# Kernel optimization log

Hardware: AMD Instinct MI355X
Metric: run time of the kernel (lower is better)

The kernel has to match this reference:

```python
import jax, jax.numpy as jnp
import numpy as np

B, S, H, NH = 2, 2048, 1024, 16
HD = H // NH
SCALE = float(H) ** 0.5  # note: source scales by sqrt(hidden_dim), not sqrt(head_dim)
EPS = 1e-5


def setup_inputs() -> dict:
    key = jax.random.key(0)
    ks = jax.random.split(key, 16)
    s = 0.02
    return {
        "q": jax.random.normal(ks[0], (B, S, H), jnp.float32),
        "k": jax.random.normal(ks[1], (B, S, H), jnp.float32),
        "v": jax.random.normal(ks[2], (B, S, H), jnp.float32),
        "mask": jax.random.randint(ks[3], (B, 1, S, S), 0, 2, jnp.int32),
        "Wq": jax.random.normal(ks[4], (H, H), jnp.float32) * s,
        "bq": jnp.zeros((H,), jnp.float32),
        "Wk": jax.random.normal(ks[5], (H, H), jnp.float32) * s,
        "bk": jnp.zeros((H,), jnp.float32),
        "Wv": jax.random.normal(ks[6], (H, H), jnp.float32) * s,
        "bv": jnp.zeros((H,), jnp.float32),
        "Wfc": jax.random.normal(ks[7], (H, H), jnp.float32) * s,
        "bfc": jnp.zeros((H,), jnp.float32),
        "gamma": jnp.ones((H,), jnp.float32),
        "beta": jnp.zeros((H,), jnp.float32),
    }


def reference(q, k, v, mask, Wq, bq, Wk, bk, Wv, bv, Wfc, bfc, gamma, beta):
    residual = q
    qh = (q @ Wq + bq).reshape(B, S, NH, HD)
    kh = (k @ Wk + bk).reshape(B, S, NH, HD)
    vh = (v @ Wv + bv).reshape(B, S, NH, HD)
    # full [B, NH, S, S] score matrix, as in the source
    energy = jnp.einsum('nqhd,nkhd->nhqk', qh, kh)
    energy = jnp.where(mask == 0, jnp.float32(-1e9), energy)
    attn = jax.nn.softmax(energy / SCALE, axis=3)  # dropout p=0.0 -> identity
    out = jnp.einsum('nhqk,nkhd->nqhd', attn, vh).reshape(B, S, H)
    y = out @ Wfc + bfc + residual
    mu = jnp.mean(y, axis=-1, keepdims=True)
    var = jnp.mean((y - mu) ** 2, axis=-1, keepdims=True)
    return gamma * (y - mu) / jnp.sqrt(var + EPS) + beta
```

## Files before the change

kernel.cpp:

```cpp
#include <hip/hip_runtime.h>
#include <hip/hip_bf16.h>

#define S_LEN  2048
#define HDIM   1024
#define NHEADS 16
#define HEADD  64
#define BATCH  2
#define MTOT   (BATCH * S_LEN)
#define K2EXP  0.04508422f

typedef __attribute__((ext_vector_type(8)))  __bf16 bf16x8;
typedef __attribute__((ext_vector_type(4)))  __bf16 bf16x4;
typedef __attribute__((ext_vector_type(4)))  float  f32x4;
typedef __attribute__((ext_vector_type(16))) float  f32x16;

__device__ __forceinline__ void gload16(const void* g, void* l) {
  __builtin_amdgcn_global_load_lds(
      (const __attribute__((address_space(1))) void*)g,
      (__attribute__((address_space(3))) void*)l, 16, 0, 0);
}
template<int STRIDE>
__device__ __forceinline__ bf16x8 lds_rdS(const __bf16* base, int row, int bcol) {
  const char* p = (const char*)base + row * STRIDE + (bcol ^ ((row & (STRIDE / 16 - 1)) << 4));
  return *(const bf16x8*)p;
}
__device__ __forceinline__ unsigned cvtpk_bf16(float lo, float hi) {
  unsigned r;
  asm("v_cvt_pk_bf16_f32 %0, %1, %2" : "=v"(r) : "v"(lo), "v"(hi));
  return r;
}
__device__ __forceinline__ void plswap(unsigned& a, unsigned& b) {
  asm volatile("v_permlane32_swap_b32 %0, %1" : "+v"(a), "+v"(b));
}

__global__ __launch_bounds__(256)
void prologue_kernel(const float* __restrict__ q, const float* __restrict__ k,
                     const float* __restrict__ v, const int* __restrict__ mask,
                     const float* __restrict__ Wq, const float* __restrict__ Wk,
                     const float* __restrict__ Wv, const float* __restrict__ Wfc,
                     __bf16* __restrict__ Qc, __bf16* __restrict__ Kc,
                     __bf16* __restrict__ Vc, unsigned* __restrict__ mbH,
                     __bf16* __restrict__ Wt)
{
  __shared__ float T[64][65];
  const int id = blockIdx.x;
  const int tid = threadIdx.x;
  if (id < 6144) {
    const int z = id >> 11, blk = id & 2047;
    const float* src = (z == 0) ? q : (z == 1) ? k : v;
    __bf16* dst = (z == 0) ? Qc : (z == 1) ? Kc : Vc;
    const size_t i = ((size_t)blk * 256 + tid) * 8;
    const float4 a = *(const float4*)&src[i];
    const float4 c = *(const float4*)&src[i + 4];
    bf16x8 o;
    o[0] = (__bf16)a.x; o[1] = (__bf16)a.y; o[2] = (__bf16)a.z; o[3] = (__bf16)a.w;
    o[4] = (__bf16)c.x; o[5] = (__bf16)c.y; o[6] = (__bf16)c.z; o[7] = (__bf16)c.w;
    *(bf16x8*)&dst[i] = o;
  } else if (id < 38912) {
    const size_t idx = (size_t)(id - 6144) * 256 + tid;
    const int m = mask[idx];
    const unsigned long long bal = __ballot(m != 0);
    const int lane = tid & 63;
    if ((lane & 31) == 0) {
      const int hh = lane >> 5;
      unsigned wlo = 0, whi = 0;
      #pragma unroll
      for (int j = 0; j < 16; ++j) {
        const int kvl = (j & 3) + 8 * (j >> 2) + 4 * hh;
        wlo |= (unsigned)((bal >> kvl) & 1ULL) << j;
        whi |= (unsigned)((bal >> (32 + kvl)) & 1ULL) << j;
      }
      const int b   = (int)(idx >> 22);
      const int qq  = (int)(idx >> 11) & 2047;
      const int seg = ((int)idx & 2047) >> 6;
      mbH[(((size_t)(hh * 2 + b)) * 32 + seg) * S_LEN + qq] = wlo | (whi << 16);
    }
  } else {
    const int f = id - 38912;
    const int z = f >> 8;
    const float* W = (z == 0) ? Wq : (z == 1) ? Wk : (z == 2) ? Wv : Wfc;
    const float sc = (z == 0) ? K2EXP : 1.0f;
    __bf16* O = Wt + (size_t)z * HDIM * HDIM;
    const int k0 = ((f >> 4) & 15) * 64, n0 = (f & 15) * 64;
    const int r  = tid >> 4;
    const int c4 = (tid & 15) * 4;
    #pragma unroll
    for (int p = 0; p < 4; ++p) {
      const int row = r + p * 16;
      const float4 vv = *(const float4*)&W[(size_t)(k0 + row) * HDIM + n0 + c4];
      T[row][c4 + 0] = vv.x; T[row][c4 + 1] = vv.y;
      T[row][c4 + 2] = vv.z; T[row][c4 + 3] = vv.w;
    }
    __syncthreads();
    #pragma unroll
    for (int p = 0; p < 4; ++p) {
      const int n = r + p * 16;
      bf16x4 o;
      #pragma unroll
      for (int i = 0; i < 4; ++i) o[i] = (__bf16)(T[c4 + i][n] * sc);
      *(bf16x4*)&O[(size_t)(n0 + n) * HDIM + k0 + c4] = o;
    }
  }
}

template<int MODE, int BMT>
__device__ __forceinline__ void gemm_body(
    __bf16* As, __bf16* Bs,
    const __bf16* __restrict__ A, const __bf16* __restrict__ Wt,
    const float* __restrict__ bias, float bscale,
    const float* __restrict__ resid,
    __bf16* __restrict__ Ob, float* __restrict__ Of, __bf16* __restrict__ Vtg)
{
  constexpr int AI = BMT / 32;
  const int tid = threadIdx.x, lane = tid & 63, w = tid >> 6;
  const int fr = lane & 15, k8 = (lane >> 4) * 8;
  const int wr = w >> 1, wc = w & 1;
  const int f   = blockIdx.x + gridDim.x * blockIdx.y;
  const int cpx = (gridDim.x * gridDim.y) >> 3;
  const int fs  = (f & 7) * cpx + (f >> 3);
  const int m0 = (fs / gridDim.x) * BMT, n0 = (fs % gridDim.x) * 128;
  const int srow8 = lane >> 3, slot = lane & 7;

  f32x4 acc[AI][4] = {};

  #define G_STAGE(kt, bf)                                                    \
    {                                                                        \
      _Pragma("unroll")                                                      \
      for (int c = 0; c < AI; ++c) {                                         \
        const int ra = w * (BMT / 4) + c * 8 + srow8;                        \
        gload16(&A[(size_t)(m0 + ra) * HDIM + (kt) * 64 + ((slot ^ (ra & 7)) * 8)], \
                (void*)&As[((bf) * BMT + ra) * 64]);                         \
      }                                                                      \
      _Pragma("unroll")                                                      \
      for (int c = 0; c < 4; ++c) {                                          \
        const int rb = w * 32 + c * 8 + srow8;                               \
        gload16(&Wt[(size_t)(n0 + rb) * HDIM + (kt) * 64 + ((slot ^ (rb & 7)) * 8)], \
                (void*)&Bs[((bf) * 128 + rb) * 64]);                         \
      }                                                                      \
    }

  #define G_COMPUTE(bf)                                                      \
    {                                                                        \
      _Pragma("unroll")                                                      \
      for (int kk = 0; kk < 64; kk += 32) {                                  \
        bf16x8 a[AI], b[4];                                                  \
        _Pragma("unroll")                                                    \
        for (int i = 0; i < AI; ++i)                                         \
          a[i] = lds_rdS<128>(&As[(bf) * BMT * 64], wr * (BMT / 2) + i * 16 + fr, (kk + k8) * 2); \
        _Pragma("unroll")                                                    \
        for (int j = 0; j < 4; ++j)                                          \
          b[j] = lds_rdS<128>(&Bs[(bf) * 128 * 64], wc * 64 + j * 16 + fr, (kk + k8) * 2); \
        _Pragma("unroll")                                                    \
        for (int i = 0; i < AI; ++i)                                         \
          _Pragma("unroll")                                                  \
          for (int j = 0; j < 4; ++j)                                        \
            acc[i][j] = __builtin_amdgcn_mfma_f32_16x16x32_bf16(a[i], b[j], acc[i][j], 0, 0, 0); \
      }                                                                      \
    }

  G_STAGE(0, 0)
  for (int kt = 0; kt < 15; ++kt) {
    G_STAGE(kt + 1, (kt + 1) & 1)
    if constexpr (BMT == 128) asm volatile("s_waitcnt vmcnt(8)" ::: "memory");
    else                      asm volatile("s_waitcnt vmcnt(6)" ::: "memory");
    __builtin_amdgcn_s_barrier();
    __builtin_amdgcn_sched_barrier(0);
    __builtin_amdgcn_s_setprio(1);
    G_COMPUTE(kt & 1)
    __builtin_amdgcn_s_setprio(0);
    __builtin_amdgcn_sched_barrier(0);
    __builtin_amdgcn_s_barrier();
  }
  asm volatile("s_waitcnt vmcnt(0)" ::: "memory");
  __builtin_amdgcn_s_barrier();
  G_COMPUTE(1)

  const int rg = (lane >> 4) * 4;
  #pragma unroll
  for (int i = 0; i < AI; ++i) {
    #pragma unroll
    for (int j = 0; j < 4; ++j) {
      const int col = n0 + wc * 64 + j * 16 + fr;
      if constexpr (MODE == 2) {
        const int h = col >> 6, hd = col & 63;
        const int row = m0 + wr * (BMT / 2) + i * 16 + rg;
        const int bq = row >> 11, qq = row & 2047;
        bf16x4 o;
        #pragma unroll
        for (int r = 0; r < 4; ++r) o[r] = (__bf16)(acc[i][j][r] + bias[col]);
        *(bf16x4*)&Vtg[(((size_t)bq * NHEADS + h) * HEADD + hd) * S_LEN + qq] = o;
      } else {
        #pragma unroll
        for (int r = 0; r < 4; ++r) {
          const int row = m0 + wr * (BMT / 2) + i * 16 + rg + r;
          if constexpr (MODE == 0) {
            Ob[(size_t)row * HDIM + col] = (__bf16)(acc[i][j][r] + bias[col] * bscale);
          } else {
            Of[(size_t)row * HDIM + col] =
                acc[i][j][r] + bias[col] + resid[(size_t)row * HDIM + col];
          }
        }
      }
    }
  }
  #undef G_STAGE
  #undef G_COMPUTE
}

__global__ __launch_bounds__(256)
void qkv_kernel(const __bf16* __restrict__ Qc, const __bf16* __restrict__ Kc,
                const __bf16* __restrict__ Vc, const __bf16* __restrict__ Wt,
                const float* __restrict__ bq, const float* __restrict__ bk,
                const float* __restrict__ bv,
                __bf16* __restrict__ Qb, __bf16* __restrict__ Kb,
                __bf16* __restrict__ Vtg)
{
  __shared__ __bf16 smem[2 * 128 * 64 * 2];
  __bf16* As = smem;
  __bf16* Bs = smem + 2 * 128 * 64;
  const int z = blockIdx.z;
  if (z == 2) {
    gemm_body<2, 128>(As, Bs, Vc, Wt + (size_t)2 * HDIM * HDIM, bv, 1.0f,
                      nullptr, nullptr, nullptr, Vtg);
  } else {
    gemm_body<0, 128>(As, Bs, z ? Kc : Qc, Wt + (size_t)z * HDIM * HDIM,
                      z ? bk : bq, z ? 1.0f : K2EXP, nullptr,
                      z ? Kb : Qb, nullptr, nullptr);
  }
}

__global__ __launch_bounds__(256)
void fc_kernel(const __bf16* __restrict__ A, const __bf16* __restrict__ Wt,
               const float* __restrict__ bias, const float* __restrict__ resid,
               float* __restrict__ Of)
{
  __shared__ __bf16 smem[2 * 64 * 64 + 2 * 128 * 64];
  __bf16* As = smem;
  __bf16* Bs = smem + 2 * 64 * 64;
  gemm_body<1, 64>(As, Bs, A, Wt + (size_t)3 * HDIM * HDIM, bias, 1.0f, resid,
                   nullptr, Of, nullptr);
}

__global__ __launch_bounds__(512)
void attn_kernel(const __bf16* __restrict__ Qb, const __bf16* __restrict__ Kb,
                 const __bf16* __restrict__ Vtg, const unsigned* __restrict__ mbH,
                 __bf16* __restrict__ AO)
{
  __shared__ __align__(16) char smem[32768];
  __bf16 (*Ks)[64][64] = (__bf16(*)[64][64])smem;
  __bf16 (*Vt)[64][64] = (__bf16(*)[64][64])(smem + 16384);

  const int bh = blockIdx.x, b = bh >> 4, h = bh & 15;
  const int tid = threadIdx.x, lane = tid & 63, w = tid >> 6;
  const int fr = lane & 31, hi = lane >> 5;
  const int qt = w >> 1, kvh = w & 1;
  const int qw = blockIdx.y * 128 + qt * 32;
  const int q  = qw + fr;

  bf16x8 qf[4];
  #pragma unroll
  for (int st = 0; st < 4; ++st)
    qf[st] = *(const bf16x8*)&Qb[((size_t)b * S_LEN + q) * HDIM + h * HEADD + st * 16 + hi * 8];

  const int srl = w * 8 + (lane >> 3);
  const int ssw = ((lane & 7) ^ (srl & 7)) * 8;
  const __bf16* ksrc = Kb  + ((size_t)b * S_LEN + srl) * HDIM + h * HEADD + ssw;
  const __bf16* vsrc = Vtg + ((size_t)bh * HEADD + srl) * S_LEN + ssw;
  const unsigned* tbl = mbH + ((size_t)(hi * 2 + b) * 32) * S_LEN + q;

  bf16x8 ones;
  #pragma unroll
  for (int e = 0; e < 8; ++e) ones[e] = (__bf16)1.0f;

  f32x16 o0 = {}, o1 = {}, l_acc = {};
  unsigned mv, nm = 0;

  mv = tbl[0];
  gload16(ksrc, (void*)&Ks[0][w * 8][0]);
  gload16(vsrc, (void*)&Vt[0][w * 8][0]);

  for (int t = 0; t < 32; ++t) {
    const int buf = t & 1;
    __builtin_amdgcn_s_barrier();
    if (t < 31) {
      nm = tbl[(size_t)(t + 1) * S_LEN];
      gload16(ksrc + (size_t)(t + 1) * 64 * HDIM, (void*)&Ks[buf ^ 1][w * 8][0]);
      gload16(vsrc + (size_t)(t + 1) * 64,        (void*)&Vt[buf ^ 1][w * 8][0]);
      asm volatile("s_waitcnt vmcnt(3)" ::: "memory");
    } else {
      asm volatile("s_waitcnt vmcnt(0)" ::: "memory");
    }
    __builtin_amdgcn_sched_barrier(0);

    const __bf16* Kbuf = &Ks[buf][0][0];
    const __bf16* Vbuf = &Vt[buf][0][0];

    f32x16 s = {};
    __builtin_amdgcn_s_setprio(1);
    #pragma unroll
    for (int st = 0; st < 4; ++st)
      s = __builtin_amdgcn_mfma_f32_32x32x16_bf16(
          lds_rdS<128>(Kbuf, kvh * 32 + fr, st * 32 + hi * 16), qf[st], s, 0, 0, 0);
    __builtin_amdgcn_s_setprio(0);

    float pp[16];
    #pragma unroll
    for (int j = 0; j < 16; ++j) {
      const float e = __builtin_amdgcn_exp2f(s[j]);
      const unsigned a = (unsigned)__builtin_amdgcn_sbfe(mv, j + 16 * kvh, 1);
      pp[j] = __uint_as_float(a & __float_as_uint(e));
    }

    bf16x8 pa[2];
    #pragma unroll
    for (int g = 0; g < 2; ++g) {
      const int o = g * 8;
      unsigned x  = cvtpk_bf16(pp[o + 0], pp[o + 1]);
      unsigned x2 = cvtpk_bf16(pp[o + 2], pp[o + 3]);
      unsigned y  = cvtpk_bf16(pp[o + 4], pp[o + 5]);
      unsigned y2 = cvtpk_bf16(pp[o + 6], pp[o + 7]);
      plswap(x, y);
      plswap(x2, y2);
      union { unsigned u[4]; bf16x8 v; } uu;
      uu.u[0] = x; uu.u[1] = x2; uu.u[2] = y; uu.u[3] = y2;
      pa[g] = uu.v;
    }

    __builtin_amdgcn_s_setprio(1);
    #pragma unroll
    for (int g = 0; g < 2; ++g) {
      const int bcol = kvh * 64 + g * 32 + hi * 16;
      l_acc = __builtin_amdgcn_mfma_f32_32x32x16_bf16(pa[g], ones, l_acc, 0, 0, 0);
      o0 = __builtin_amdgcn_mfma_f32_32x32x16_bf16(
          pa[g], lds_rdS<128>(Vbuf, fr,      bcol), o0, 0, 0, 0);
      o1 = __builtin_amdgcn_mfma_f32_32x32x16_bf16(
          pa[g], lds_rdS<128>(Vbuf, 32 + fr, bcol), o1, 0, 0, 0);
    }
    __builtin_amdgcn_s_setprio(0);

    mv = nm;
  }

  float* sh = (float*)smem;
  #pragma unroll
  for (int ph = 0; ph < 2; ++ph) {
    __builtin_amdgcn_s_barrier();
    if ((qt >> 1) == ph && kvh) {
      float* p = sh + ((size_t)(qt & 1) * 64 + lane) * 48;
      #pragma unroll
      for (int j = 0; j < 16; ++j) { p[j] = o0[j]; p[16 + j] = o1[j]; p[32 + j] = l_acc[j]; }
    }
    __builtin_amdgcn_s_barrier();
    if ((qt >> 1) == ph && !kvh) {
      const float* p = sh + ((size_t)(qt & 1) * 64 + lane) * 48;
      #pragma unroll
      for (int g = 0; g < 4; ++g) {
        #pragma unroll
        for (int r = 0; r < 4; ++r) {
          const int j = g * 4 + r;
          const float inv = __builtin_amdgcn_rcpf(l_acc[j] + p[32 + j]);
          const int qq = qw + g * 8 + hi * 4 + r;
          AO[((size_t)b * S_LEN + qq) * HDIM + h * HEADD + fr]      =
              (__bf16)((o0[j] + p[j]) * inv);
          AO[((size_t)b * S_LEN + qq) * HDIM + h * HEADD + 32 + fr] =
              (__bf16)((o1[j] + p[16 + j]) * inv);
        }
      }
    }
  }
}

__global__ __launch_bounds__(256)
void ln_kernel(float* __restrict__ y, const float* __restrict__ gamma,
               const float* __restrict__ beta)
{
  __shared__ float red[8];
  const int tid = threadIdx.x;
  float* p = y + (size_t)blockIdx.x * HDIM;

  float4 vv = *(const float4*)&p[tid * 4];
  float s  = vv.x + vv.y + vv.z + vv.w;
  float ss = vv.x * vv.x + vv.y * vv.y + vv.z * vv.z + vv.w * vv.w;
  #pragma unroll
  for (int d = 1; d < 64; d <<= 1) {
    s  += __shfl_xor(s, d);
    ss += __shfl_xor(ss, d);
  }
  const int wid = tid >> 6;
  if ((tid & 63) == 0) { red[wid * 2] = s; red[wid * 2 + 1] = ss; }
  __syncthreads();
  s  = red[0] + red[2] + red[4] + red[6];
  ss = red[1] + red[3] + red[5] + red[7];
  const float mean = s * (1.0f / HDIM);
  const float var  = ss * (1.0f / HDIM) - mean * mean;
  const float inv  = rsqrtf(var + 1e-5f);

  const float4 g  = *(const float4*)&gamma[tid * 4];
  const float4 bt = *(const float4*)&beta[tid * 4];
  vv.x = (vv.x - mean) * inv * g.x + bt.x;
  vv.y = (vv.y - mean) * inv * g.y + bt.y;
  vv.z = (vv.z - mean) * inv * g.z + bt.z;
  vv.w = (vv.w - mean) * inv * g.w + bt.w;
  *(float4*)&p[tid * 4] = vv;
}

extern "C" void kernel_launch(void* const* d_in, const int* in_sizes, int n_in,
                              void* d_out, int out_size, void* d_ws, size_t ws_size,
                              hipStream_t stream) {
  const float* q     = (const float*)d_in[0];
  const float* k     = (const float*)d_in[1];
  const float* v     = (const float*)d_in[2];
  const int*   mask  = (const int*)  d_in[3];
  const float* Wq    = (const float*)d_in[4];
  const float* bq    = (const float*)d_in[5];
  const float* Wk    = (const float*)d_in[6];
  const float* bk    = (const float*)d_in[7];
  const float* Wv    = (const float*)d_in[8];
  const float* bv    = (const float*)d_in[9];
  const float* Wfc   = (const float*)d_in[10];
  const float* bfc   = (const float*)d_in[11];
  const float* gamma = (const float*)d_in[12];
  const float* beta  = (const float*)d_in[13];
  float* out = (float*)d_out;

  char* ws = (char*)d_ws;
  const size_t MB16 = (size_t)MTOT * HDIM * 2;
  unsigned* mbH = (unsigned*)ws;
  __bf16* Wt  = (__bf16*)(ws + (1u << 20));
  __bf16* Qc  = (__bf16*)(ws + (1u << 20) + 4 * (size_t)HDIM * HDIM * 2);
  __bf16* Kc  = (__bf16*)((char*)Qc + MB16);
  __bf16* Vc  = (__bf16*)((char*)Kc + MB16);
  __bf16* Qb  = (__bf16*)((char*)Vc + MB16);
  __bf16* Kb  = (__bf16*)((char*)Qb + MB16);
  __bf16* Vtg = (__bf16*)((char*)Kb + MB16);
  __bf16* AO  = Kc;

  const dim3 blk(256);

  prologue_kernel<<<dim3(39936), blk, 0, stream>>>(
      q, k, v, mask, Wq, Wk, Wv, Wfc, Qc, Kc, Vc, mbH, Wt);

  qkv_kernel<<<dim3(HDIM / 128, MTOT / 128, 3), blk, 0, stream>>>(
      Qc, Kc, Vc, Wt, bq, bk, bv, Qb, Kb, Vtg);

  attn_kernel<<<dim3(BATCH * NHEADS, S_LEN / 128), dim3(512), 0, stream>>>(
      Qb, Kb, Vtg, mbH, AO);

  fc_kernel<<<dim3(HDIM / 128, MTOT / 64), blk, 0, stream>>>(
      AO, Wt, bfc, q, out);

  ln_kernel<<<dim3(MTOT), blk, 0, stream>>>(out, gamma, beta);
}
```

Measured before the change: 154.8 us.

## Triple-buffer K/V tiles and software-pipeline QK^T one tile ahead in attention

The attention loop moves from double to triple buffering of K and V tiles in LDS, prefetching two tiles ahead, and computes the QK^T scores for the next tile while the exp and PV step runs on the current one. This is meant to overlap MFMA work with the exp/convert VALU work and hide global-load latency. The final cross-wave reduction is also restructured into a single phase with a transposed LDS layout, which removes barriers. In exchange the kernel uses more LDS (48KB) and more registers for the extra score accumulator, which may lower occupancy.

```diff
diff --git a/kernel.cpp b/kernel.cpp
--- a/kernel.cpp
+++ b/kernel.cpp
@@ -246,9 +246,9 @@
                  const __bf16* __restrict__ Vtg, const unsigned* __restrict__ mbH,
                  __bf16* __restrict__ AO)
 {
-  __shared__ __align__(16) char smem[32768];
+  __shared__ __align__(16) char smem[49152];
   __bf16 (*Ks)[64][64] = (__bf16(*)[64][64])smem;
-  __bf16 (*Vt)[64][64] = (__bf16(*)[64][64])(smem + 16384);
+  __bf16 (*Vt)[64][64] = (__bf16(*)[64][64])(smem + 24576);
 
   const int bh = blockIdx.x, b = bh >> 4, h = bh & 15;
   const int tid = threadIdx.x, lane = tid & 63, w = tid >> 6;
@@ -273,44 +273,56 @@
   for (int e = 0; e < 8; ++e) ones[e] = (__bf16)1.0f;
 
   f32x16 o0 = {}, o1 = {}, l_acc = {};
-  unsigned mv, nm = 0;
-
-  mv = tbl[0];
-  gload16(ksrc, (void*)&Ks[0][w * 8][0]);
-  gload16(vsrc, (void*)&Vt[0][w * 8][0]);
-
+
+  unsigned mv  = tbl[0];
+  unsigned nmA = tbl[S_LEN];
+  unsigned nmB = 0;
+  gload16(ksrc,            (void*)&Ks[0][w * 8][0]);
+  gload16(vsrc,            (void*)&Vt[0][w * 8][0]);
+  gload16(ksrc + 64 * HDIM, (void*)&Ks[1][w * 8][0]);
+  gload16(vsrc + 64,        (void*)&Vt[1][w * 8][0]);
+  asm volatile("s_waitcnt vmcnt(2)" ::: "memory");
+  __builtin_amdgcn_s_barrier();
+
+  f32x16 s_cur = {};
+  {
+    const __bf16* Kb0 = &Ks[0][0][0];
+    #pragma unroll
+    for (int st = 0; st < 4; ++st)
+      s_cur = __builtin_amdgcn_mfma_f32_32x32x16_bf16(
+          lds_rdS<128>(Kb0, kvh * 32 + fr, st * 32 + hi * 16), qf[st], s_cur, 0, 0, 0);
+  }
+
+  int c0 = 0, c1 = 1, c2 = 2;
   for (int t = 0; t < 32; ++t) {
-    const int buf = t & 1;
+    asm volatile("s_waitcnt vmcnt(0)" ::: "memory");
     __builtin_amdgcn_s_barrier();
+    __builtin_amdgcn_sched_barrier(0);
+
+    if (t < 30) {
+      gload16(ksrc + (size_t)(t + 2) * 64 * HDIM, (void*)&Ks[c2][w * 8][0]);
+      gload16(vsrc + (size_t)(t + 2) * 64,        (void*)&Vt[c2][w * 8][0]);
+      nmB = tbl[(size_t)(t + 2) * S_LEN];
+    }
+
+    f32x16 s_nxt = {};
     if (t < 31) {
-      nm = tbl[(size_t)(t + 1) * S_LEN];
-      gload16(ksrc + (size_t)(t + 1) * 64 * HDIM, (void*)&Ks[buf ^ 1][w * 8][0]);
-      gload16(vsrc + (size_t)(t + 1) * 64,        (void*)&Vt[buf ^ 1][w * 8][0]);
-      asm volatile("s_waitcnt vmcnt(3)" ::: "memory");
-    } else {
-      asm volatile("s_waitcnt vmcnt(0)" ::: "memory");
-    }
-    __builtin_amdgcn_sched_barrier(0);
-
-    const __bf16* Kbuf = &Ks[buf][0][0];
-    const __bf16* Vbuf = &Vt[buf][0][0];
-
-    f32x16 s = {};
-    __builtin_amdgcn_s_setprio(1);
-    #pragma unroll
-    for (int st = 0; st < 4; ++st)
-      s = __builtin_amdgcn_mfma_f32_32x32x16_bf16(
-          lds_rdS<128>(Kbuf, kvh * 32 + fr, st * 32 + hi * 16), qf[st], s, 0, 0, 0);
-    __builtin_amdgcn_s_setprio(0);
+      const __bf16* Kbn = &Ks[c1][0][0];
+      __builtin_amdgcn_s_setprio(1);
+      #pragma unroll
+      for (int st = 0; st < 4; ++st)
+        s_nxt = __builtin_amdgcn_mfma_f32_32x32x16_bf16(
+            lds_rdS<128>(Kbn, kvh * 32 + fr, st * 32 + hi * 16), qf[st], s_nxt, 0, 0, 0);
+      __builtin_amdgcn_s_setprio(0);
+    }
 
     float pp[16];
     #pragma unroll
     for (int j = 0; j < 16; ++j) {
-      const float e = __builtin_amdgcn_exp2f(s[j]);
+      const float e = __builtin_amdgcn_exp2f(s_cur[j]);
       const unsigned a = (unsigned)__builtin_amdgcn_sbfe(mv, j + 16 * kvh, 1);
       pp[j] = __uint_as_float(a & __float_as_uint(e));
     }
-
     bf16x8 pa[2];
     #pragma unroll
     for (int g = 0; g < 2; ++g) {
@@ -326,45 +338,50 @@
       pa[g] = uu.v;
     }
 
-    __builtin_amdgcn_s_setprio(1);
-    #pragma unroll
-    for (int g = 0; g < 2; ++g) {
-      const int bcol = kvh * 64 + g * 32 + hi * 16;
-      l_acc = __builtin_amdgcn_mfma_f32_32x32x16_bf16(pa[g], ones, l_acc, 0, 0, 0);
-      o0 = __builtin_amdgcn_mfma_f32_32x32x16_bf16(
-          pa[g], lds_rdS<128>(Vbuf, fr,      bcol), o0, 0, 0, 0);
-      o1 = __builtin_amdgcn_mfma_f32_32x32x16_bf16(
-          pa[g], lds_rdS<128>(Vbuf, 32 + fr, bcol), o1, 0, 0, 0);
-    }
-    __builtin_amdgcn_s_setprio(0);
-
-    mv = nm;
-  }
-
+    {
+      const __bf16* Vbc = &Vt[c0][0][0];
+      __builtin_amdgcn_s_setprio(1);
+      #pragma unroll
+      for (int g = 0; g < 2; ++g) {
+        const int bcol = kvh * 64 + g * 32 + hi * 16;
+        l_acc = __builtin_amdgcn_mfma_f32_32x32x16_bf16(pa[g], ones, l_acc, 0, 0, 0);
+        o0 = __builtin_amdgcn_mfma_f32_32x32x16_bf16(
+            pa[g], lds_rdS<128>(Vbc, fr,      bcol), o0, 0, 0, 0);
+        o1 = __builtin_amdgcn_mfma_f32_32x32x16_bf16(
+            pa[g], lds_rdS<128>(Vbc, 32 + fr, bcol), o1, 0, 0, 0);
+      }
+      __builtin_amdgcn_s_setprio(0);
+    }
+
+    mv = nmA; nmA = nmB;
+    s_cur = s_nxt;
+    const int tmp = c0; c0 = c1; c1 = c2; c2 = tmp;
+  }
+
+  __builtin_amdgcn_s_barrier();
   float* sh = (float*)smem;
-  #pragma unroll
-  for (int ph = 0; ph < 2; ++ph) {
-    __builtin_amdgcn_s_barrier();
-    if ((qt >> 1) == ph && kvh) {
-      float* p = sh + ((size_t)(qt & 1) * 64 + lane) * 48;
+  const int li = qt * 64 + lane;
+  if (kvh) {
+    #pragma unroll
+    for (int j = 0; j < 16; ++j) {
+      sh[(j)      * 256 + li] = o0[j];
+      sh[(16 + j) * 256 + li] = o1[j];
+      sh[(32 + j) * 256 + li] = l_acc[j];
+    }
+  }
+  __builtin_amdgcn_s_barrier();
+  if (!kvh) {
+    #pragma unroll
+    for (int g = 0; g < 4; ++g) {
       #pragma unroll
-      for (int j = 0; j < 16; ++j) { p[j] = o0[j]; p[16 + j] = o1[j]; p[32 + j] = l_acc[j]; }
-    }
-    __builtin_amdgcn_s_barrier();
-    if ((qt >> 1) == ph && !kvh) {
-      const float* p = sh + ((size_t)(qt & 1) * 64 + lane) * 48;
-      #pragma unroll
-      for (int g = 0; g < 4; ++g) {
-        #pragma unroll
-        for (int r = 0; r < 4; ++r) {
-          const int j = g * 4 + r;
-          const float inv = __builtin_amdgcn_rcpf(l_acc[j] + p[32 + j]);
-          const int qq = qw + g * 8 + hi * 4 + r;
-          AO[((size_t)b * S_LEN + qq) * HDIM + h * HEADD + fr]      =
-              (__bf16)((o0[j] + p[j]) * inv);
-          AO[((size_t)b * S_LEN + qq) * HDIM + h * HEADD + 32 + fr] =
-              (__bf16)((o1[j] + p[16 + j]) * inv);
-        }
+      for (int r = 0; r < 4; ++r) {
+        const int j = g * 4 + r;
+        const float inv = __builtin_amdgcn_rcpf(l_acc[j] + sh[(32 + j) * 256 + li]);
+        const int qq = qw + g * 8 + hi * 4 + r;
+        AO[((size_t)b * S_LEN + qq) * HDIM + h * HEADD + fr]      =
+            (__bf16)((o0[j] + sh[(j) * 256 + li]) * inv);
+        AO[((size_t)b * S_LEN + qq) * HDIM + h * HEADD + 32 + fr] =
+            (__bf16)((o1[j] + sh[(16 + j) * 256 + li]) * inv);
       }
     }
   }
```

Result: no change. 155.2 us (+0.3%).
